# Performance work log

Hardware: AMD Instinct MI355X
Metric: run time of the kernel (lower is better)

The kernel has to match this reference:

```python
import jax, jax.numpy as jnp
import numpy as np

B_SZ, L, D, N, H = 2, 2048, 1024, 16, 128

def celu(x):
    # F.celu with alpha=1: max(0,x) + min(0, exp(x)-1)
    return jnp.where(x > 0, x, jnp.expm1(x))

def setup_inputs() -> dict:
    key = jax.random.key(0)
    ks = jax.random.split(key, 16)
    s = lambda fan_in: 1.0 / np.sqrt(fan_in)
    inp = {
        "x": jax.random.normal(ks[0], (B_SZ, L, D), jnp.float32),
        # fc1: d->d, fc2/fc3: d->n
        "W1": jax.random.normal(ks[1], (D, D), jnp.float32) * s(D),
        "b1": jnp.zeros((D,), jnp.float32),
        "W2": jax.random.normal(ks[2], (D, N), jnp.float32) * s(D),
        "b2": jnp.zeros((N,), jnp.float32),
        "W3": jax.random.normal(ks[3], (D, N), jnp.float32) * s(D),
        "b3": jnp.zeros((N,), jnp.float32),
        # lift_fn: Linear(d,128) -> relu -> Linear(128,d) -> tanh
        "Wl1": jax.random.normal(ks[4], (D, H), jnp.float32) * s(D),
        "bl1": jnp.zeros((H,), jnp.float32),
        "Wl2": jax.random.normal(ks[5], (H, D), jnp.float32) * s(H),
        "bl2": jnp.zeros((D,), jnp.float32),
        # fc_net: Linear(2d,128) -> relu -> (dropout, eval: identity) -> Linear(128,d)
        "Wf1": jax.random.normal(ks[6], (2 * D, H), jnp.float32) * s(2 * D),
        "bf1": jnp.zeros((H,), jnp.float32),
        "Wf2": jax.random.normal(ks[7], (H, D), jnp.float32) * s(H),
        "bf2": jnp.zeros((D,), jnp.float32),
        "state_init": jnp.zeros((1, D, N), jnp.float32),
        # kaiming_normal_ on (d, n): std = sqrt(2 / fan_in), fan_in = n
        "A": jax.random.normal(ks[8], (D, N), jnp.float32) * np.sqrt(2.0 / N),
    }
    return inp

def reference(x, W1, b1, W2, b2, W3, b3, Wl1, bl1, Wl2, bl2, Wf1, bf1, Wf2, bf2, state_init, A):
    b = x.shape[0]
    # lift_fn
    lifted = jnp.tanh(jax.nn.relu(x @ Wl1 + bl1) @ Wl2 + bl2)          # [b,l,d]
    combined = jnp.concatenate([x, lifted], axis=-1)                    # [b,l,2d]
    x_trans = jax.nn.relu(combined @ Wf1 + bf1) @ Wf2 + bf2             # [b,l,d]
    h_prev = jnp.broadcast_to(state_init, (b,) + state_init.shape[1:])  # [b,d,n]
    Bm = x_trans @ W2 + b2                                              # [b,l,n]
    Cm = x_trans @ W3 + b3                                              # [b,l,n]
    delta = jax.nn.softplus(x_trans @ W1 + b1)                          # [b,l,d]
    # discretization: bldn outer products
    dB = delta[..., :, None] * Bm[..., None, :]                         # [b,l,d,n]
    dA = jnp.exp(-celu(delta[..., :, None] * A[None, None]))            # [b,l,d,n]
    h_new = dA * h_prev[:, None] + x_trans[..., None] * dB              # [b,l,d,n]
    output = jnp.einsum('bln,bldn->bld', Cm, h_new)                     # [b,l,d]
    last_h_state = h_new[:, -1]                                         # [b,d,n]
    return (output, last_h_state)
```

## Files before the change

### kernel.cpp

```cpp
#include <hip/hip_runtime.h>
#include <cmath>

#define B_SZ 2
#define LSEQ 2048
#define DDIM 1024
#define NDIM 16
#define HDIM 128
#define MROWS (B_SZ * LSEQ)
#define NBIG (DDIM + 2 * NDIM)
#define NPAD 1088

typedef __bf16 bf16x8 __attribute__((ext_vector_type(8)));
typedef __bf16 bf16x4 __attribute__((ext_vector_type(4)));
typedef float f32x4 __attribute__((ext_vector_type(4)));

__device__ __forceinline__ void glds16(const __bf16* g, __bf16* l) {
    __builtin_amdgcn_global_load_lds(
        (const __attribute__((address_space(1))) unsigned int*)g,
        (__attribute__((address_space(3))) unsigned int*)l, 16, 0, 0);
}

__device__ __forceinline__ int slot_xt(int d) { return (d >> 4) * 32 + (d & 15); }
__device__ __forceinline__ int slot_de(int d) { return (d >> 4) * 32 + 16 + (d & 15); }

__device__ __forceinline__ void tcast_tile(const float* __restrict__ in,
                                           __bf16* __restrict__ out, int K, int N,
                                           int bx, int by, float (*t)[33]) {
    int tx = threadIdx.x & 31, ty = threadIdx.x >> 5;
    int n0 = bx * 32, k0 = by * 32;
    #pragma unroll
    for (int i = 0; i < 4; ++i) {
        int k = k0 + ty + i * 8, n = n0 + tx;
        t[ty + i * 8][tx] = (k < K && n < N) ? in[(size_t)k * N + n] : 0.f;
    }
    __syncthreads();
    #pragma unroll
    for (int i = 0; i < 4; ++i) {
        int n = n0 + ty + i * 8, k = k0 + tx;
        if (n < N && k < K) out[(size_t)n * K + k] = (__bf16)t[tx][ty + i * 8];
    }
}

__device__ __forceinline__ void tcast_pair_tile(const float* __restrict__ in,
                                                __bf16* __restrict__ out,
                                                int bx, int by, float (*t)[33]) {
    int tx = threadIdx.x & 31, ty = threadIdx.x >> 5;
    int n0 = bx * 32, k0 = by * 32;
    #pragma unroll
    for (int i = 0; i < 4; ++i) {
        int k = k0 + ty + i * 8, n = n0 + tx;
        t[ty + i * 8][tx] = in[(size_t)k * 1024 + n];
    }
    __syncthreads();
    #pragma unroll
    for (int i = 0; i < 4; ++i) {
        int n = n0 + ty + i * 8, k = k0 + tx;
        out[(size_t)slot_xt(n) * 128 + k] = (__bf16)t[tx][ty + i * 8];
    }
}

__global__ __launch_bounds__(256) void pack_all(
    const float* W1, const float* W2, const float* W3, const float* Wl1,
    const float* Wl2, const float* Wf1, const float* Wf2,
    const float* bf2, const float* h0,
    __bf16* WbigT, __bf16* WaT, __bf16* Wf1bT, __bf16* Wl2T, __bf16* WpairT,
    __bf16* Wf2c, float* bias_pair, unsigned* h0mask) {
    __shared__ float t[32][33];
    const int b = blockIdx.x;
    const int tid = threadIdx.x;
    if (b < 1024) {
        tcast_tile(W1, WbigT, 1024, 1024, b & 31, b >> 5, t);
    } else if (b < 1152) {
        int i = b - 1024; tcast_tile(Wl1, WaT, 1024, 128, i & 3, i >> 2, t);
    } else if (b < 1280) {
        int i = b - 1152; tcast_tile(Wf1, WaT + 128 * 1024, 1024, 128, i & 3, i >> 2, t);
    } else if (b < 1408) {
        int i = b - 1280;
        tcast_tile(Wf1 + (size_t)1024 * 128, Wf1bT, 1024, 128, i & 3, i >> 2, t);
    } else if (b < 1536) {
        int i = b - 1408; tcast_tile(Wl2, Wl2T, 128, 1024, i & 31, i >> 5, t);
    } else if (b < 1664) {
        int i = b - 1536; tcast_pair_tile(Wf2, WpairT, i & 31, i >> 5, t);
    } else if (b < 1696) {
        int i = b - 1664; tcast_tile(W2, WbigT + (size_t)1024 * 1024, 1024, 16, 0, i, t);
    } else if (b < 1728) {
        int i = b - 1696; tcast_tile(W3, WbigT + (size_t)1040 * 1024, 1024, 16, 0, i, t);
    } else if (b < 1732) {
        int i = (b - 1728) * 256 + tid;
        bias_pair[slot_xt(i)] = bf2[i];
    } else if (b < 1764) {
        int i = (b - 1732) * 256 + tid;
        #pragma unroll
        for (int r = 0; r < 4; ++r) {
            int e = i + r * 8192;
            if (e < 32 * 1024) WbigT[(size_t)1056 * 1024 + e] = (__bf16)0.f;
        }
    } else if (b < 1796) {
        int id = (b - 1764) * 256 + tid;
        #pragma unroll
        for (int j = 0; j < 4; ++j) {
            int e = id + j * 8192;
            float4 v = ((const float4*)Wf2)[e];
            bf16x4 o2 = {(__bf16)v.x, (__bf16)v.y, (__bf16)v.z, (__bf16)v.w};
            ((bf16x4*)Wf2c)[e] = o2;
        }
    } else {
        __shared__ unsigned sm[32];
        if (tid < 32) sm[tid] = 0u;
        __syncthreads();
        unsigned nib = 0;
        #pragma unroll
        for (int j = 0; j < 4; ++j) {
            int d = tid * 4 + j;
            const uint4* hu = (const uint4*)(h0 + d * NDIM);
            uint4 a0 = hu[0], a1 = hu[1], a2 = hu[2], a3 = hu[3];
            unsigned nz = a0.x | a0.y | a0.z | a0.w | a1.x | a1.y | a1.z | a1.w |
                          a2.x | a2.y | a2.z | a2.w | a3.x | a3.y | a3.z | a3.w;
            if (nz) nib |= (1u << j);
        }
        if (nib) atomicOr(&sm[(tid * 4) >> 5], nib << ((tid * 4) & 31));
        __syncthreads();
        if (tid < 32) h0mask[tid] = sm[tid];
    }
}

template <int BM, int BN, int BK, int NBUF, int ACT, bool ADD_PREV, bool GUARDN, bool AF32>
__device__ __forceinline__ void gemm_core(
    const void* Av, int lda, const __bf16* __restrict__ Bt, int ldb, int Ntot,
    const float* __restrict__ bias, const __bf16* __restrict__ prev, int ldp,
    __bf16* __restrict__ C, int ldc, int K, int bm, int bn,
    __bf16* As, __bf16* Bs) {
    constexpr int WM = BM / 2, WN = BN / 2, FM = WM / 16, FN = WN / 16;
    constexpr int ASZ = BM * BK, BSZ = BN * BK;
    constexpr int CPR = BK / 8;
    constexpr int NH = BK / 32;
    const int tid = threadIdx.x;
    const int lane = tid & 63, w = tid >> 6;
    const int wr = w >> 1, wc = w & 1;
    const int g = lane >> 4, lr = lane & 15;
    const __bf16* A16 = (const __bf16*)Av;
    const float* A32 = (const float*)Av;

    auto stage = [&](int buf, int k0) {
        #pragma unroll
        for (int i = 0; i < BM * BK / 2048; ++i) {
            int D = i * 256 + tid;
            int row = D / CPR, pos = D % CPR, c = pos ^ (row & 7);
            if constexpr (AF32) {
                const float* s = &A32[(size_t)(bm + row) * lda + k0 + c * 8];
                float4 v0 = *(const float4*)s;
                float4 v1 = *(const float4*)(s + 4);
                bf16x8 pk = {(__bf16)v0.x, (__bf16)v0.y, (__bf16)v0.z, (__bf16)v0.w,
                             (__bf16)v1.x, (__bf16)v1.y, (__bf16)v1.z, (__bf16)v1.w};
                *(bf16x8*)&As[buf * ASZ + row * BK + pos * 8] = pk;
            } else {
                glds16(&A16[(size_t)(bm + row) * lda + k0 + c * 8],
                       &As[buf * ASZ + (i * 256 + w * 64) * 8]);
            }
        }
        #pragma unroll
        for (int i = 0; i < BN * BK / 2048; ++i) {
            int D = i * 256 + tid;
            int row = D / CPR, pos = D % CPR, c = pos ^ (row & 7);
            glds16(&Bt[(size_t)(bn + row) * ldb + k0 + c * 8],
                   &Bs[buf * BSZ + (i * 256 + w * 64) * 8]);
        }
    };

    f32x4 acc[FM][FN] = {};
    const int x7 = lr & 7;
    int ca[NH];
    #pragma unroll
    for (int h = 0; h < NH; ++h) ca[h] = ((h * 4 + g) ^ x7) * 8;
    const int arow0 = wr * WM + lr;
    const int brow0 = wc * WN + lr;

    const int nt = K / BK;
    stage(0, 0);
    __syncthreads();
    for (int t = 0; t < nt; ++t) {
        if (NBUF == 2 && t + 1 < nt) stage((t + 1) & 1, (t + 1) * BK);
        const __bf16* Ab = &As[(NBUF == 2 ? (t & 1) : 0) * ASZ];
        const __bf16* Bb = &Bs[(NBUF == 2 ? (t & 1) : 0) * BSZ];
        bf16x8 af[FM][NH], bfr[FN][NH];
        #pragma unroll
        for (int m = 0; m < FM; ++m)
            #pragma unroll
            for (int h = 0; h < NH; ++h)
                af[m][h] = *(const bf16x8*)&Ab[(arow0 + m * 16) * BK + ca[h]];
        #pragma unroll
        for (int n = 0; n < FN; ++n)
            #pragma unroll
            for (int h = 0; h < NH; ++h)
                bfr[n][h] = *(const bf16x8*)&Bb[(brow0 + n * 16) * BK + ca[h]];
        #pragma unroll
        for (int h = 0; h < NH; ++h)
            #pragma unroll
            for (int m = 0; m < FM; ++m)
                #pragma unroll
                for (int n = 0; n < FN; ++n)
                    acc[m][n] = __builtin_amdgcn_mfma_f32_16x16x32_bf16(
                        af[m][h], bfr[n][h], acc[m][n], 0, 0, 0);
        __syncthreads();
    }

    #pragma unroll
    for (int m = 0; m < FM; ++m) {
        #pragma unroll
        for (int n = 0; n < FN; ++n) {
            #pragma unroll
            for (int r = 0; r < 4; ++r) {
                int grow = bm + wr * WM + m * 16 + g * 4 + r;
                int gcol = bn + wc * WN + n * 16 + lr;
                if (!GUARDN || gcol < Ntot) {
                    float v = acc[m][n][r];
                    int orow = grow;
                    if (ACT == 1) {
                        v += bias[gcol];
                        if (ADD_PREV) v += (float)prev[(size_t)grow * ldp + gcol];
                        v = fmaxf(v, 0.f);
                    } else if (ACT == 2) {
                        v += bias[gcol];
                        float e = __expf(2.f * v);
                        v = 1.f - 2.f * __builtin_amdgcn_rcpf(e + 1.f);
                    } else if (ACT == 4) {
                        if (gcol < HDIM) v = fmaxf(v + bias[gcol], 0.f);
                    } else if (ACT == 7) {
                        orow = (grow < 1024) ? slot_de(grow) : 2048 + (grow - 1024);
                    }
                    C[(size_t)orow * ldc + gcol] = (__bf16)v;
                }
            }
        }
    }
}

template <int BM, int BN, int BK, int NBUF, int ACT, bool ADD_PREV, bool GUARDN>
__global__ __launch_bounds__(256) void mm(const __bf16* __restrict__ A, int lda,
                                          const __bf16* __restrict__ Bt, int ldb, int Ntot,
                                          const float* __restrict__ bias,
                                          const __bf16* __restrict__ prev, int ldp,
                                          __bf16* __restrict__ C, int ldc, int K, int nbx) {
    __shared__ __bf16 As[NBUF * BM * BK];
    __shared__ __bf16 Bs[NBUF * BN * BK];
    const int NB = gridDim.x;
    const int aid = ((NB & 7) == 0)
                        ? (blockIdx.x & 7) * (NB >> 3) + (blockIdx.x >> 3)
                        : blockIdx.x;
    const int bn = (aid % nbx) * BN, bm = (aid / nbx) * BM;
    gemm_core<BM, BN, BK, NBUF, ACT, ADD_PREV, GUARDN, false>(
        A, lda, Bt, ldb, Ntot, bias, prev, ldp, C, ldc, K, bm, bn, As, Bs);
}

__global__ __launch_bounds__(256) void stage2_k(
    const float* __restrict__ x, const __bf16* __restrict__ WaT,
    const __bf16* __restrict__ WbigT, const __bf16* __restrict__ Wf2c,
    const float* __restrict__ bf2, const float* __restrict__ b1,
    const float* __restrict__ b2, const float* __restrict__ b3,
    const float* __restrict__ bl1,
    __bf16* __restrict__ tmp12, __bf16* __restrict__ WpairT,
    float* __restrict__ bias_pair) {
    __shared__ __bf16 As[8192];
    __shared__ __bf16 Bs[16384];
    const int b = blockIdx.x;
    if (b < 512) {
        const int aid = (b & 7) * 64 + (b >> 3);
        const int bn = (aid & 3) * 64, bm = (aid >> 2) * 32;
        gemm_core<32, 64, 128, 2, 4, false, false, true>(
            x, DDIM, WaT, 1024, 256, bl1, nullptr, 0, tmp12, 256, 1024, bm, bn, As, Bs);
    } else if (b < 546) {
        const int aid = b - 512;
        const int bn = (aid & 1) * 64, bm = (aid >> 1) * 64;
        gemm_core<64, 64, 64, 2, 7, false, false, false>(
            WbigT, 1024, Wf2c, 1024, 128, nullptr, nullptr, 0,
            WpairT, 128, 1024, bm, bn, As, Bs);
    } else {
        const int n = (b - 546) * 4 + (threadIdx.x >> 6);
        const int lane = threadIdx.x & 63;
        const __bf16* wr = WbigT + (size_t)n * 1024 + lane * 16;
        float s = 0.f;
        #pragma unroll
        for (int i = 0; i < 2; ++i) {
            bf16x8 wv = *(const bf16x8*)&wr[i * 8];
            float4 f0 = *(const float4*)&bf2[lane * 16 + i * 8];
            float4 f1 = *(const float4*)&bf2[lane * 16 + i * 8 + 4];
            s += (float)wv[0] * f0.x + (float)wv[1] * f0.y + (float)wv[2] * f0.z +
                 (float)wv[3] * f0.w + (float)wv[4] * f1.x + (float)wv[5] * f1.y +
                 (float)wv[6] * f1.z + (float)wv[7] * f1.w;
        }
        #pragma unroll
        for (int off = 32; off; off >>= 1) s += __shfl_down(s, off);
        if (lane == 0) {
            float base = (n < DDIM) ? b1[n]
                       : (n < DDIM + NDIM) ? b2[n - DDIM] : b3[n - DDIM - NDIM];
            int sl = (n < DDIM) ? slot_de(n) : 2048 + (n - DDIM);
            bias_pair[sl] = base + s;
        }
    }
}

__global__ __launch_bounds__(256) void mm_pairs(
    const __bf16* __restrict__ tmp2, const __bf16* __restrict__ WpairT,
    const float* __restrict__ bias_pair,
    const float* __restrict__ Amat, const float* __restrict__ h0,
    const unsigned* __restrict__ h0mask,
    float* __restrict__ out, float* __restrict__ last_h) {
    constexpr int ASZ = 128 * 64, BSZ = 64 * 64;
    __shared__ __bf16 As[2 * ASZ];
    __shared__ __bf16 Bs[2 * BSZ];
    const int NB = gridDim.x;
    const int aid = (blockIdx.x & 7) * (NB >> 3) + (blockIdx.x >> 3);
    const int bn = (aid & 31) * 64, bm = (aid >> 5) * 128;
    const int tid = threadIdx.x;
    const int lane = tid & 63, w = tid >> 6;
    const int wr = w >> 1, wc = w & 1;
    const int g = lane >> 4, lr = lane & 15;

    auto stage = [&](int buf, int k0) {
        #pragma unroll
        for (int i = 0; i < 4; ++i) {
            int D = i * 256 + tid;
            int row = D >> 3, pos = D & 7, c = pos ^ (row & 7);
            glds16(&tmp2[(size_t)(bm + row) * 128 + k0 + c * 8],
                   &As[buf * ASZ + (i * 256 + w * 64) * 8]);
        }
        #pragma unroll
        for (int i = 0; i < 2; ++i) {
            int D = i * 256 + tid;
            int row = D >> 3, pos = D & 7, c = pos ^ (row & 7);
            glds16(&WpairT[(size_t)(bn + row) * 128 + k0 + c * 8],
                   &Bs[buf * BSZ + (i * 256 + w * 64) * 8]);
        }
    };

    f32x4 acc[4][2] = {};
    const int x7 = lr & 7;
    const int ca[2] = {(g ^ x7) * 8, ((4 + g) ^ x7) * 8};
    const int arow0 = wr * 64 + lr, brow0 = wc * 32 + lr;
    stage(0, 0);
    __syncthreads();
    #pragma unroll
    for (int t = 0; t < 2; ++t) {
        if (t == 0) stage(1, 64);
        const __bf16* Ab = &As[t * ASZ];
        const __bf16* Bb = &Bs[t * BSZ];
        bf16x8 af[4][2], bfr[2][2];
        #pragma unroll
        for (int m = 0; m < 4; ++m)
            #pragma unroll
            for (int h = 0; h < 2; ++h)
                af[m][h] = *(const bf16x8*)&Ab[(arow0 + m * 16) * 64 + ca[h]];
        #pragma unroll
        for (int n = 0; n < 2; ++n)
            #pragma unroll
            for (int h = 0; h < 2; ++h)
                bfr[n][h] = *(const bf16x8*)&Bb[(brow0 + n * 16) * 64 + ca[h]];
        #pragma unroll
        for (int h = 0; h < 2; ++h)
            #pragma unroll
            for (int m = 0; m < 4; ++m)
                #pragma unroll
                for (int n = 0; n < 2; ++n)
                    acc[m][n] = __builtin_amdgcn_mfma_f32_16x16x32_bf16(
                        af[m][h], bfr[n][h], acc[m][n], 0, 0, 0);
        __syncthreads();
    }

    {
        int row = tid >> 3, pos = tid & 7, c = pos ^ (row & 7);
        #pragma unroll
        for (int t2 = 0; t2 < 2; ++t2)
            glds16(&WpairT[(size_t)(2048 + row) * 128 + t2 * 64 + c * 8],
                   &Bs[t2 * 2048 + w * 512]);
    }
    __syncthreads();
    f32x4 accB[2] = {}, accC[2] = {};
    #pragma unroll
    for (int t2 = 0; t2 < 2; ++t2) {
        const __bf16* Ab = &As[t2 * ASZ];
        #pragma unroll
        for (int h = 0; h < 2; ++h) {
            bf16x8 bB = *(const bf16x8*)&Bs[t2 * 2048 + lr * 64 + ca[h]];
            bf16x8 bC = *(const bf16x8*)&Bs[t2 * 2048 + (16 + lr) * 64 + ca[h]];
            #pragma unroll
            for (int m2 = 0; m2 < 2; ++m2) {
                bf16x8 a2 = *(const bf16x8*)&Ab[(w * 32 + m2 * 16 + lr) * 64 + ca[h]];
                accB[m2] = __builtin_amdgcn_mfma_f32_16x16x32_bf16(a2, bB, accB[m2], 0, 0, 0);
                accC[m2] = __builtin_amdgcn_mfma_f32_16x16x32_bf16(a2, bC, accC[m2], 0, 0, 0);
            }
        }
    }
    __syncthreads();
    float* sCB = (float*)As;
    __bf16* sBC = &Bs[BSZ];
    const float bB_ = bias_pair[2048 + lr], bC_ = bias_pair[2064 + lr];
    #pragma unroll
    for (int m2 = 0; m2 < 2; ++m2) {
        #pragma unroll
        for (int r = 0; r < 4; ++r) {
            int lrow = w * 32 + m2 * 16 + g * 4 + r;
            float vB = accB[m2][r] + bB_;
            float vC = accC[m2][r] + bC_;
            sBC[lrow * 32 + lr] = (__bf16)vB;
            sBC[lrow * 32 + 16 + lr] = (__bf16)vC;
            float p = vB * vC;
            #pragma unroll
            for (int m3 = 1; m3 < 16; m3 <<= 1) p += __shfl_xor(p, m3);
            if (lr == 0) sCB[lrow] = p;
        }
    }
    __syncthreads();

    const int d = ((bn + wc * 32) >> 1) + lr;
    const float bx_ = bias_pair[bn + wc * 32 + lr];
    const float bd_ = bias_pair[bn + wc * 32 + 16 + lr];
    const bool msk = (h0mask[d >> 5] >> (d & 31)) & 1u;
    #pragma unroll
    for (int m = 0; m < 4; ++m) {
        #pragma unroll
        for (int r = 0; r < 4; ++r) {
            const int lrow = wr * 64 + m * 16 + g * 4 + r;
            const int row = bm + lrow;
            const float xt = acc[m][0][r] + bx_;
            const float dr = acc[m][1][r] + bd_;
            const float e = __expf(-fabsf(dr));
            const float de = fmaxf(dr, 0.f) + __logf(1.f + e);
            const float xd = xt * de;
            float res = xd * sCB[lrow];
            const bool is_last = (row & (LSEQ - 1)) == (LSEQ - 1);
            if (msk) {
                float s = 0.f;
                #pragma unroll
                for (int n = 0; n < NDIM; ++n) {
                    float z = de * Amat[d * NDIM + n];
                    float c2 = (z > 0.f) ? z : __expf(z) - 1.f;
                    float da = __expf(-c2);
                    float h0v = h0[d * NDIM + n];
                    s += (float)sBC[lrow * 32 + 16 + n] * da * h0v;
                    if (is_last)
                        last_h[(((size_t)(row >> 11)) * DDIM + d) * NDIM + n] =
                            da * h0v + xd * (float)sBC[lrow * 32 + n];
                }
                res += s;
            } else if (is_last) {
                #pragma unroll
                for (int n = 0; n < NDIM; ++n)
                    last_h[(((size_t)(row >> 11)) * DDIM + d) * NDIM + n] =
                        xd * (float)sBC[lrow * 32 + n];
            }
            out[(size_t)row * DDIM + d] = res;
        }
    }
}

extern "C" void kernel_launch(void* const* d_in, const int* in_sizes, int n_in,
                              void* d_out, int out_size, void* d_ws, size_t ws_size,
                              hipStream_t stream) {
    const float* x   = (const float*)d_in[0];
    const float* W1  = (const float*)d_in[1];
    const float* b1  = (const float*)d_in[2];
    const float* W2  = (const float*)d_in[3];
    const float* b2  = (const float*)d_in[4];
    const float* W3  = (const float*)d_in[5];
    const float* b3  = (const float*)d_in[6];
    const float* Wl1 = (const float*)d_in[7];
    const float* bl1 = (const float*)d_in[8];
    const float* Wl2 = (const float*)d_in[9];
    const float* bl2 = (const float*)d_in[10];
    const float* Wf1 = (const float*)d_in[11];
    const float* bf1 = (const float*)d_in[12];
    const float* Wf2 = (const float*)d_in[13];
    const float* bf2 = (const float*)d_in[14];
    const float* h0  = (const float*)d_in[15];
    const float* Amat= (const float*)d_in[16];

    float* out    = (float*)d_out;
    float* last_h = (float*)d_out + (size_t)MROWS * DDIM;

    __bf16* wsb = (__bf16*)d_ws;
    size_t o = 0;
    auto alloc = [&](size_t n) { __bf16* p = wsb + o; o += n; return p; };
    __bf16* WaT    = alloc(256 * 1024);
    __bf16* Wf1bT  = alloc(128 * 1024);
    __bf16* Wl2T   = alloc(1024 * 128);
    __bf16* WbigT  = alloc((size_t)NPAD * 1024);
    __bf16* WpairT = alloc(2112 * 128);
    __bf16* Wf2c   = alloc(128 * 1024);
    __bf16* tmp12  = alloc((size_t)MROWS * 256);
    __bf16* lifted = alloc((size_t)MROWS * DDIM);
    __bf16* tmp2   = alloc((size_t)MROWS * HDIM);
    float*  bias_pair = (float*)(wsb + o); o += 2 * 2112;
    unsigned* h0mask = (unsigned*)(wsb + o);

    pack_all<<<dim3(1797), 256, 0, stream>>>(W1, W2, W3, Wl1, Wl2, Wf1, Wf2,
                                             bf2, h0,
                                             WbigT, WaT, Wf1bT, Wl2T, WpairT,
                                             Wf2c, bias_pair, h0mask);
    stage2_k<<<dim3(810), 256, 0, stream>>>(x, WaT, WbigT, Wf2c, bf2, b1, b2, b3,
                                            bl1, tmp12, WpairT, bias_pair);
    mm<64, 64, 128, 1, 2, false, false><<<dim3(16 * 64), 256, 0, stream>>>(
        tmp12, 256, Wl2T, 128, 1024, bl2, nullptr, 0, lifted, DDIM, 128, 16);
    mm<32, 32, 256, 2, 1, true, false><<<dim3(4 * 128), 256, 0, stream>>>(
        lifted, DDIM, Wf1bT, 1024, 128, bf1, tmp12 + 128, 256, tmp2, HDIM, 1024, 4);
    mm_pairs<<<dim3(32 * 32), 256, 0, stream>>>(tmp2, WpairT, bias_pair,
                                                Amat, h0, h0mask, out, last_h);
}
```

Baseline: 54.10 us.

## Fuse lift second layer and fc_net first layer into one kernel

```diff
diff --git a/kernel.cpp b/kernel.cpp
--- a/kernel.cpp
+++ b/kernel.cpp
@@ -235,23 +235,6 @@
     }
 }
 
-template <int BM, int BN, int BK, int NBUF, int ACT, bool ADD_PREV, bool GUARDN>
-__global__ __launch_bounds__(256) void mm(const __bf16* __restrict__ A, int lda,
-                                          const __bf16* __restrict__ Bt, int ldb, int Ntot,
-                                          const float* __restrict__ bias,
-                                          const __bf16* __restrict__ prev, int ldp,
-                                          __bf16* __restrict__ C, int ldc, int K, int nbx) {
-    __shared__ __bf16 As[NBUF * BM * BK];
-    __shared__ __bf16 Bs[NBUF * BN * BK];
-    const int NB = gridDim.x;
-    const int aid = ((NB & 7) == 0)
-                        ? (blockIdx.x & 7) * (NB >> 3) + (blockIdx.x >> 3)
-                        : blockIdx.x;
-    const int bn = (aid % nbx) * BN, bm = (aid / nbx) * BM;
-    gemm_core<BM, BN, BK, NBUF, ACT, ADD_PREV, GUARDN, false>(
-        A, lda, Bt, ldb, Ntot, bias, prev, ldp, C, ldc, K, bm, bn, As, Bs);
-}
-
 __global__ __launch_bounds__(256) void stage2_k(
     const float* __restrict__ x, const __bf16* __restrict__ WaT,
     const __bf16* __restrict__ WbigT, const __bf16* __restrict__ Wf2c,
@@ -268,14 +251,14 @@
         const int bn = (aid & 3) * 64, bm = (aid >> 2) * 32;
         gemm_core<32, 64, 128, 2, 4, false, false, true>(
             x, DDIM, WaT, 1024, 256, bl1, nullptr, 0, tmp12, 256, 1024, bm, bn, As, Bs);
-    } else if (b < 546) {
+    } else if (b < 580) {
         const int aid = b - 512;
-        const int bn = (aid & 1) * 64, bm = (aid >> 1) * 64;
-        gemm_core<64, 64, 64, 2, 7, false, false, false>(
+        const int bm = (aid >> 1) * 32, bn = (aid & 1) * 64;
+        gemm_core<32, 64, 128, 2, 7, false, false, false>(
             WbigT, 1024, Wf2c, 1024, 128, nullptr, nullptr, 0,
             WpairT, 128, 1024, bm, bn, As, Bs);
     } else {
-        const int n = (b - 546) * 4 + (threadIdx.x >> 6);
+        const int n = (b - 580) * 4 + (threadIdx.x >> 6);
         const int lane = threadIdx.x & 63;
         const __bf16* wr = WbigT + (size_t)n * 1024 + lane * 16;
         float s = 0.f;
@@ -296,6 +279,89 @@
             int sl = (n < DDIM) ? slot_de(n) : 2048 + (n - DDIM);
             bias_pair[sl] = base + s;
         }
+    }
+}
+
+__global__ __launch_bounds__(512) void g23_k(
+    const __bf16* __restrict__ tmp12, const __bf16* __restrict__ Wl2T,
+    const __bf16* __restrict__ Wf1bT, const float* __restrict__ bl2,
+    const float* __restrict__ bf1, __bf16* __restrict__ tmp2) {
+    __shared__ __bf16 T1[2048];
+    __shared__ __bf16 LS[2048];
+    __shared__ __bf16 B1[2][16384];
+    __shared__ __bf16 B2[2][16384];
+    const int tid = threadIdx.x;
+    const int lane = tid & 63, w = tid >> 6;
+    const int g = lane >> 4, lr = lane & 15;
+    const int x7 = lr & 7;
+    const int bm = blockIdx.x * 16;
+
+    if (tid < 256) {
+        int row = tid >> 4, pos = tid & 15, c = pos ^ (row & 7);
+        glds16(&tmp12[(size_t)(bm + row) * 256 + c * 8], &T1[w * 512]);
+    }
+    auto stageB = [&](int buf, int kc) {
+        #pragma unroll
+        for (int i = 0; i < 4; ++i) {
+            int D = i * 512 + tid;
+            int row = D >> 4, pos = D & 15, c = pos ^ (row & 7);
+            glds16(&Wl2T[(size_t)(kc + row) * 128 + c * 8],
+                   &B1[buf][(i * 512 + w * 64) * 8]);
+            glds16(&Wf1bT[(size_t)row * 1024 + kc + c * 8],
+                   &B2[buf][(i * 512 + w * 64) * 8]);
+        }
+    };
+
+    int ca[4];
+    #pragma unroll
+    for (int h = 0; h < 4; ++h) ca[h] = ((h * 4 + g) ^ x7) * 8;
+    const int col = w * 16 + lr;
+    const int brow = col * 128;
+
+    stageB(0, 0);
+    __syncthreads();
+    bf16x8 a1[4];
+    #pragma unroll
+    for (int h = 0; h < 4; ++h) a1[h] = *(const bf16x8*)&T1[lr * 128 + ca[h]];
+
+    f32x4 acc2 = {};
+    for (int t = 0; t < 8; ++t) {
+        if (t + 1 < 8) stageB((t + 1) & 1, (t + 1) * 128);
+        const __bf16* b1b = B1[t & 1];
+        const __bf16* b2b = B2[t & 1];
+        f32x4 acc1 = {};
+        #pragma unroll
+        for (int h = 0; h < 4; ++h) {
+            bf16x8 bf = *(const bf16x8*)&b1b[brow + ca[h]];
+            acc1 = __builtin_amdgcn_mfma_f32_16x16x32_bf16(a1[h], bf, acc1, 0, 0, 0);
+        }
+        const float bl = bl2[t * 128 + col];
+        const int chunk = col >> 3, cin = col & 7;
+        #pragma unroll
+        for (int r = 0; r < 4; ++r) {
+            float v = acc1[r] + bl;
+            float e = __expf(2.f * v);
+            v = 1.f - 2.f * __builtin_amdgcn_rcpf(e + 1.f);
+            int row = g * 4 + r;
+            LS[row * 128 + ((chunk ^ (row & 7)) << 3) + cin] = (__bf16)v;
+        }
+        __syncthreads();
+        #pragma unroll
+        for (int h = 0; h < 4; ++h) {
+            bf16x8 a2 = *(const bf16x8*)&LS[lr * 128 + ca[h]];
+            bf16x8 bf = *(const bf16x8*)&b2b[brow + ca[h]];
+            acc2 = __builtin_amdgcn_mfma_f32_16x16x32_bf16(a2, bf, acc2, 0, 0, 0);
+        }
+        __syncthreads();
+    }
+
+    const float bfv = bf1[col];
+    #pragma unroll
+    for (int r = 0; r < 4; ++r) {
+        const int row = g * 4 + r;
+        float v = acc2[r] + bfv + (float)tmp12[(size_t)(bm + row) * 256 + 128 + col];
+        v = fmaxf(v, 0.f);
+        tmp2[(size_t)(bm + row) * 128 + col] = (__bf16)v;
     }
 }
 
@@ -487,7 +553,6 @@
     __bf16* WpairT = alloc(2112 * 128);
     __bf16* Wf2c   = alloc(128 * 1024);
     __bf16* tmp12  = alloc((size_t)MROWS * 256);
-    __bf16* lifted = alloc((size_t)MROWS * DDIM);
     __bf16* tmp2   = alloc((size_t)MROWS * HDIM);
     float*  bias_pair = (float*)(wsb + o); o += 2 * 2112;
     unsigned* h0mask = (unsigned*)(wsb + o);
@@ -496,12 +561,9 @@
                                              bf2, h0,
                                              WbigT, WaT, Wf1bT, Wl2T, WpairT,
                                              Wf2c, bias_pair, h0mask);
-    stage2_k<<<dim3(810), 256, 0, stream>>>(x, WaT, WbigT, Wf2c, bf2, b1, b2, b3,
+    stage2_k<<<dim3(844), 256, 0, stream>>>(x, WaT, WbigT, Wf2c, bf2, b1, b2, b3,
                                             bl1, tmp12, WpairT, bias_pair);
-    mm<64, 64, 128, 1, 2, false, false><<<dim3(16 * 64), 256, 0, stream>>>(
-        tmp12, 256, Wl2T, 128, 1024, bl2, nullptr, 0, lifted, DDIM, 128, 16);
-    mm<32, 32, 256, 2, 1, true, false><<<dim3(4 * 128), 256, 0, stream>>>(
-        lifted, DDIM, Wf1bT, 1024, 128, bf1, tmp12 + 128, 256, tmp2, HDIM, 1024, 4);
+    g23_k<<<dim3(256), 512, 0, stream>>>(tmp12, Wl2T, Wf1bT, bl2, bf1, tmp2);
     mm_pairs<<<dim3(32 * 32), 256, 0, stream>>>(tmp2, WpairT, bias_pair,
                                                 Amat, h0, h0mask, out, last_h);
 }
```

Result: faster. 51.28 us (-5.2%).
